# Kernel tuning notes

Measured on AMD Instinct MI355X. Metric: run time of the kernel, lower is better.

The kernel has to match this reference:

```python
import jax, jax.numpy as jnp
import numpy as np

N_NODES = 100000


def gcn_conv(x, W, b, src, dst, num_nodes):
    """PyG GCNConv: self-loops + symmetric norm + linear + scatter-add."""
    loop = jnp.arange(num_nodes, dtype=src.dtype)
    s = jnp.concatenate([src, loop])  # [E+N]
    d = jnp.concatenate([dst, loop])  # [E+N]
    # degree on destination column (edge_weight = 1)
    deg = jax.ops.segment_sum(jnp.ones_like(d, dtype=x.dtype), d,
                              num_segments=num_nodes)
    dinv = jnp.where(deg > 0, jax.lax.rsqrt(deg), 0.0)
    norm = dinv[s] * dinv[d]  # [E+N]
    h = x @ W  # [N, out] project before aggregation
    msg = h[s] * norm[:, None]  # gather + normalize
    out = jax.ops.segment_sum(msg, d, num_segments=num_nodes)  # scatter-add
    return out + b


def setup_inputs() -> dict:
    key = jax.random.key(0)
    k_x, k_e, k_w1, k_b1, k_w2, k_b2 = jax.random.split(key, 6)
    in_channels, hidden, out_dim = 128, 64, 2
    n_edges = 3200000
    x = jax.random.normal(k_x, (N_NODES, in_channels), dtype=jnp.float32)
    edge_index = jax.random.randint(k_e, (2, n_edges), 0, N_NODES, dtype=jnp.int64)
    # Glorot-style init for linear weights, zero bias (PyG default)
    W1 = jax.random.normal(k_w1, (in_channels, hidden), dtype=jnp.float32) * (1.0 / np.sqrt(in_channels))
    b1 = jnp.zeros((hidden,), dtype=jnp.float32)
    W2 = jax.random.normal(k_w2, (hidden, out_dim), dtype=jnp.float32) * (1.0 / np.sqrt(hidden))
    b2 = jnp.zeros((out_dim,), dtype=jnp.float32)
    return {"x": x, "edge_index": edge_index, "W1": W1, "b1": b1, "W2": W2, "b2": b2}


def reference(x, edge_index, W1, b1, W2, b2):
    src, dst = edge_index[0], edge_index[1]
    h = gcn_conv(x, W1, b1, src, dst, N_NODES)
    h = jax.nn.relu(h)
    # dropout(p=0.3) is identity in eval mode
    return gcn_conv(h, W2, b2, src, dst, N_NODES)
```

## Files before the change

kernel.cpp:

```cpp
#include <hip/hip_runtime.h>
#include <hip/hip_fp16.h>

#define IN_CH 128
#define HID 64
#define CHUNK1 16384
#define GBITS 8
#define SCAN_CHUNK 8192

typedef _Float16 h2 __attribute__((ext_vector_type(2)));
__device__ __forceinline__ h2 asH2(unsigned u) {
    union { unsigned u; h2 h; } x; x.u = u; return x.h;
}
__device__ __forceinline__ unsigned packH2(float a, float b) {
    union { unsigned u; h2 h; } x;
    x.h.x = (_Float16)a; x.h.y = (_Float16)b;
    return x.u;
}

__global__ __launch_bounds__(512) void k_p1count(const int* __restrict__ dst,
                                                 int* __restrict__ C,
                                                 int E, int G, int NB1) {
    __shared__ int lcnt[512];
    int t = threadIdx.x;
    for (int i = t; i < G; i += 512) lcnt[i] = 0;
    __syncthreads();
    int lo = blockIdx.x * CHUNK1;
    int hi = min(E, lo + CHUNK1);
    for (int e = lo + t; e < hi; e += 512) {
        int d = __builtin_nontemporal_load(dst + e);
        atomicAdd(&lcnt[d >> GBITS], 1);
    }
    __syncthreads();
    for (int g = t; g < G; g += 512) C[(size_t)g * NB1 + blockIdx.x] = lcnt[g];
}

__global__ __launch_bounds__(256) void k_scan_blocksum(const int* __restrict__ a,
                                                       int* __restrict__ bsum, int M) {
    int t = threadIdx.x;
    int base = blockIdx.x * SCAN_CHUNK + t * 32;
    int s = 0;
#pragma unroll
    for (int q = 0; q < 8; ++q) {
        int b = base + q * 4;
        if (b + 3 < M) {
            int4 v = *(const int4*)(a + b);
            s += v.x + v.y + v.z + v.w;
        } else {
            for (int i = 0; i < 4; ++i) if (b + i < M) s += a[b + i];
        }
    }
#pragma unroll
    for (int off = 32; off; off >>= 1) s += __shfl_down(s, off);
    __shared__ int ws[4];
    if ((t & 63) == 0) ws[t >> 6] = s;
    __syncthreads();
    if (t == 0) bsum[blockIdx.x] = ws[0] + ws[1] + ws[2] + ws[3];
}

__global__ __launch_bounds__(128) void k_scan_bsums(int* __restrict__ bsum, int nb) {
    __shared__ int sh[128];
    int t = threadIdx.x;
    int v = (t < nb) ? bsum[t] : 0;
    sh[t] = v;
    __syncthreads();
    for (int off = 1; off < 128; off <<= 1) {
        int u = (t >= off) ? sh[t - off] : 0;
        __syncthreads();
        sh[t] += u;
        __syncthreads();
    }
    if (t < nb) bsum[t] = (t == 0) ? 0 : sh[t - 1];
}

__global__ __launch_bounds__(256) void k_scan_apply(int* __restrict__ a,
                                                    const int* __restrict__ boff,
                                                    int M, int E) {
    int t = threadIdx.x;
    int base = blockIdx.x * SCAN_CHUNK + t * 32;
    int v[32];
    int tsum = 0;
#pragma unroll
    for (int q = 0; q < 8; ++q) {
        int b = base + q * 4;
        if (b + 3 < M) {
            int4 w = *(const int4*)(a + b);
            v[q * 4 + 0] = w.x; v[q * 4 + 1] = w.y; v[q * 4 + 2] = w.z; v[q * 4 + 3] = w.w;
        } else {
            for (int i = 0; i < 4; ++i) v[q * 4 + i] = (b + i < M) ? a[b + i] : 0;
        }
        tsum += v[q * 4] + v[q * 4 + 1] + v[q * 4 + 2] + v[q * 4 + 3];
    }
    __shared__ int sh[256];
    sh[t] = tsum;
    __syncthreads();
    for (int off = 1; off < 256; off <<= 1) {
        int u = (t >= off) ? sh[t - off] : 0;
        __syncthreads();
        sh[t] += u;
        __syncthreads();
    }
    int run = ((t == 0) ? 0 : sh[t - 1]) + boff[blockIdx.x];
#pragma unroll
    for (int q = 0; q < 8; ++q) {
        int b = base + q * 4;
        int o0 = run;            run += v[q * 4 + 0];
        int o1 = run;            run += v[q * 4 + 1];
        int o2 = run;            run += v[q * 4 + 2];
        int o3 = run;            run += v[q * 4 + 3];
        if (b + 3 < M) { *(int4*)(a + b) = make_int4(o0, o1, o2, o3); }
        else {
            if (b     < M) a[b]     = o0;
            if (b + 1 < M) a[b + 1] = o1;
            if (b + 2 < M) a[b + 2] = o2;
            if (b + 3 < M) a[b + 3] = o3;
        }
    }
    if (blockIdx.x == 0 && t == 0) a[M] = E;
}

__global__ __launch_bounds__(512) void k_p1scat(const int* __restrict__ src,
                                                const int* __restrict__ dst,
                                                const int* __restrict__ S,
                                                unsigned int* __restrict__ part,
                                                int E, int G, int NB1) {
    __shared__ int lcur[512];
    int t = threadIdx.x;
    for (int g = t; g < G; g += 512) lcur[g] = S[(size_t)g * NB1 + blockIdx.x];
    __syncthreads();
    int lo = blockIdx.x * CHUNK1;
    int hi = min(E, lo + CHUNK1);
    for (int e = lo + t; e < hi; e += 512) {
        int d = __builtin_nontemporal_load(dst + e);
        int s = __builtin_nontemporal_load(src + e);
        int pos = atomicAdd(&lcur[d >> GBITS], 1);
        part[pos] = ((unsigned)s << GBITS) | (unsigned)(d & ((1 << GBITS) - 1));
    }
}

__global__ __launch_bounds__(512) void k_p2(const unsigned int* __restrict__ part,
                                            const int* __restrict__ S,
                                            int* __restrict__ rowptr,
                                            float* __restrict__ dinv,
                                            int* __restrict__ esorted,
                                            int E, int N, int G, int NB1) {
    __shared__ int lcnt[256], lpre[256], lexc[256];
    int t = threadIdx.x;
    int g = blockIdx.x;
    int base = S[(size_t)g * NB1];
    int end  = (g == G - 1) ? E : S[(size_t)(g + 1) * NB1];
    if (t < 256) lcnt[t] = 0;
    __syncthreads();
    unsigned int  ed[18];
    unsigned char rk[18];
#pragma unroll
    for (int q = 0; q < 18; ++q) {
        int i = base + t + q * 512;
        if (i < end) {
            unsigned p = part[i];
            ed[q] = p;
            rk[q] = (unsigned char)atomicAdd(&lcnt[p & 255], 1);
        }
    }
    __syncthreads();
    int v = 0;
    if (t < 256) { v = lcnt[t]; lpre[t] = v; }
    __syncthreads();
    for (int off = 1; off < 256; off <<= 1) {
        int u = (t >= off && t < 256) ? lpre[t - off] : 0;
        __syncthreads();
        if (t < 256) lpre[t] += u;
        __syncthreads();
    }
    if (t < 256) {
        int excl = lpre[t] - v;
        lexc[t] = excl;
        int node = (g << GBITS) + t;
        if (node < N) {
            rowptr[node] = base + excl;
            dinv[node] = rsqrtf(1.0f + (float)v);
        }
    }
    if (g == 0 && t == 0) rowptr[N] = E;
    __syncthreads();
#pragma unroll
    for (int q = 0; q < 18; ++q) {
        int i = base + t + q * 512;
        if (i < end) {
            unsigned p = ed[q];
            esorted[base + lexc[p & 255] + (int)rk[q]] = (int)(p >> GBITS);
        }
    }
}

__global__ __launch_bounds__(256) void k_gemm1(const float* __restrict__ x,
                                               const float* __restrict__ W1,
                                               const float* __restrict__ dinv,
                                               __half* __restrict__ hp1h, int N) {
    __shared__ unsigned sW[64 * 64];
    __shared__ unsigned sx[16 * 64];
    const int tid = threadIdx.x;
    const int node0 = blockIdx.x * 16;

#pragma unroll
    for (int q = 0; q < 16; ++q) {
        int idx = tid + q * 256;
        int j2 = idx >> 6, k = idx & 63;
        sW[idx] = packH2(W1[(2 * j2) * HID + k], W1[(2 * j2 + 1) * HID + k]);
    }
#pragma unroll
    for (int q = 0; q < 4; ++q) {
        int idx = tid + q * 256;
        int n = idx >> 6, j2 = idx & 63;
        float2 v = *(const float2*)(x + (size_t)(node0 + n) * IN_CH + 2 * j2);
        sx[idx] = packH2(v.x, v.y);
    }
    __syncthreads();

    const int k  = tid & 63;
    const int n0 = tid >> 6;
    float a0 = 0.f, a1 = 0.f, a2 = 0.f, a3 = 0.f;
#pragma unroll 8
    for (int j2 = 0; j2 < 64; ++j2) {
        h2 w = asH2(sW[j2 * 64 + k]);
        a0 = __builtin_amdgcn_fdot2(asH2(sx[(n0     ) * 64 + j2]), w, a0, false);
        a1 = __builtin_amdgcn_fdot2(asH2(sx[(n0 +  4) * 64 + j2]), w, a1, false);
        a2 = __builtin_amdgcn_fdot2(asH2(sx[(n0 +  8) * 64 + j2]), w, a2, false);
        a3 = __builtin_amdgcn_fdot2(asH2(sx[(n0 + 12) * 64 + j2]), w, a3, false);
    }
    hp1h[(size_t)(node0 + n0     ) * HID + k] = __float2half(a0 * dinv[node0 + n0]);
    hp1h[(size_t)(node0 + n0 +  4) * HID + k] = __float2half(a1 * dinv[node0 + n0 + 4]);
    hp1h[(size_t)(node0 + n0 +  8) * HID + k] = __float2half(a2 * dinv[node0 + n0 + 8]);
    hp1h[(size_t)(node0 + n0 + 12) * HID + k] = __float2half(a3 * dinv[node0 + n0 + 12]);
}

__global__ __launch_bounds__(256) void k_agg1(const int* __restrict__ rowptr,
                                              const int* __restrict__ esorted,
                                              const __half2* __restrict__ hp1h,
                                              const float* __restrict__ dinv,
                                              const float* __restrict__ b1,
                                              const float* __restrict__ W2,
                                              float* __restrict__ hp2, int N) {
    int wid = (blockIdx.x * blockDim.x + threadIdx.x) >> 6;
    if (wid >= N) return;
    const int lane = threadIdx.x & 63;
    const int k32  = lane & 31;
    const int half = lane >> 5;
    int beg = rowptr[wid], end = rowptr[wid + 1];

    float ax = 0.f, ay = 0.f;
    int e = beg;
    for (; e + 31 < end; e += 32) {
        const int* ep = esorted + e + 16 * half;
        int s0 = ep[0],  s1 = ep[1],  s2 = ep[2],  s3 = ep[3];
        int s4 = ep[4],  s5 = ep[5],  s6 = ep[6],  s7 = ep[7];
        int s8 = ep[8],  s9 = ep[9],  sa = ep[10], sb = ep[11];
        int sc = ep[12], sd = ep[13], se = ep[14], sf = ep[15];
        __half2 g0 = hp1h[(unsigned)(s0 * 32 + k32)];
        __half2 g1 = hp1h[(unsigned)(s1 * 32 + k32)];
        __half2 g2 = hp1h[(unsigned)(s2 * 32 + k32)];
        __half2 g3 = hp1h[(unsigned)(s3 * 32 + k32)];
        __half2 g4 = hp1h[(unsigned)(s4 * 32 + k32)];
        __half2 g5 = hp1h[(unsigned)(s5 * 32 + k32)];
        __half2 g6 = hp1h[(unsigned)(s6 * 32 + k32)];
        __half2 g7 = hp1h[(unsigned)(s7 * 32 + k32)];
        __half2 g8 = hp1h[(unsigned)(s8 * 32 + k32)];
        __half2 g9 = hp1h[(unsigned)(s9 * 32 + k32)];
        __half2 ga = hp1h[(unsigned)(sa * 32 + k32)];
        __half2 gb = hp1h[(unsigned)(sb * 32 + k32)];
        __half2 gc = hp1h[(unsigned)(sc * 32 + k32)];
        __half2 gd = hp1h[(unsigned)(sd * 32 + k32)];
        __half2 ge = hp1h[(unsigned)(se * 32 + k32)];
        __half2 gf = hp1h[(unsigned)(sf * 32 + k32)];
        __half2 h0 = __hadd2(g0, g4), h1 = __hadd2(g1, g5);
        __half2 h2 = __hadd2(g2, g6), h3 = __hadd2(g3, g7);
        float2 f0 = __half22float2(__hadd2(h0, h1));
        float2 f1 = __half22float2(__hadd2(h2, h3));
        __half2 h4 = __hadd2(g8, gc), h5 = __hadd2(g9, gd);
        __half2 h6 = __hadd2(ga, ge), h7 = __hadd2(gb, gf);
        float2 f2 = __half22float2(__hadd2(h4, h5));
        float2 f3 = __half22float2(__hadd2(h6, h7));
        ax += (f0.x + f1.x) + (f2.x + f3.x);
        ay += (f0.y + f1.y) + (f2.y + f3.y);
    }
    for (; e + 15 < end; e += 16) {
        const int* ep = esorted + e + 8 * half;
        int s0 = ep[0], s1 = ep[1], s2 = ep[2], s3 = ep[3];
        int s4 = ep[4], s5 = ep[5], s6 = ep[6], s7 = ep[7];
        __half2 h0 = hp1h[(unsigned)(s0 * 32 + k32)];
        __half2 h1 = hp1h[(unsigned)(s1 * 32 + k32)];
        __half2 h2 = hp1h[(unsigned)(s2 * 32 + k32)];
        __half2 h3 = hp1h[(unsigned)(s3 * 32 + k32)];
        h0 = __hadd2(h0, hp1h[(unsigned)(s4 * 32 + k32)]);
        h1 = __hadd2(h1, hp1h[(unsigned)(s5 * 32 + k32)]);
        h2 = __hadd2(h2, hp1h[(unsigned)(s6 * 32 + k32)]);
        h3 = __hadd2(h3, hp1h[(unsigned)(s7 * 32 + k32)]);
        float2 f0 = __half22float2(__hadd2(h0, h1));
        float2 f1 = __half22float2(__hadd2(h2, h3));
        ax += f0.x + f1.x;
        ay += f0.y + f1.y;
    }
    for (; e + 1 < end; e += 2) {
        int s = esorted[e + half];
        float2 f = __half22float2(hp1h[(unsigned)(s * 32 + k32)]);
        ax += f.x;
        ay += f.y;
    }
    if (e < end) {
        int s = esorted[e];
        float2 f = __half22float2(hp1h[(unsigned)(s * 32 + k32)]);
        if (half == 0) { ax += f.x; ay += f.y; }
    }
    ax += __shfl_xor(ax, 32);
    ay += __shfl_xor(ay, 32);

    float2 fs = __half22float2(hp1h[(unsigned)(wid * 32 + k32)]);
    ax += fs.x;
    ay += fs.y;

    float dj = dinv[wid];
    float2 bb = *(const float2*)(b1 + 2 * k32);
    float h0 = fmaxf(fmaf(dj, ax, bb.x), 0.0f);
    float h1 = fmaxf(fmaf(dj, ay, bb.y), 0.0f);
    float4 w4 = *(const float4*)(W2 + 4 * k32);
    float p0 = h0 * w4.x + h1 * w4.z;
    float p1 = h0 * w4.y + h1 * w4.w;
#pragma unroll
    for (int off = 32; off; off >>= 1) {
        p0 += __shfl_xor(p0, off);
        p1 += __shfl_xor(p1, off);
    }
    if (lane == 0) {
        hp2[(size_t)wid * 2 + 0] = p0 * 0.5f * dj;
        hp2[(size_t)wid * 2 + 1] = p1 * 0.5f * dj;
    }
}

__global__ __launch_bounds__(256) void k_agg2(const int* __restrict__ rowptr,
                                              const int* __restrict__ esorted,
                                              const float* __restrict__ hp2,
                                              const float* __restrict__ dinv,
                                              const float* __restrict__ b2,
                                              float* __restrict__ out, int N) {
    int gid = blockIdx.x * blockDim.x + threadIdx.x;
    int j = gid >> 3;
    if (j >= N) return;
    int l = gid & 7;
    int beg = rowptr[j], end = rowptr[j + 1];
    float ax = 0.f, ay = 0.f;
    for (int e = beg + l; e < end; e += 8) {
        int s = esorted[e];
        float2 v = *(const float2*)(hp2 + (size_t)s * 2);
        ax += v.x;
        ay += v.y;
    }
#pragma unroll
    for (int off = 1; off < 8; off <<= 1) {
        ax += __shfl_xor(ax, off);
        ay += __shfl_xor(ay, off);
    }
    if (l == 0) {
        float2 self = *(const float2*)(hp2 + (size_t)j * 2);
        float dj = dinv[j];
        out[(size_t)j * 2 + 0] = fmaf(dj, ax + self.x, b2[0]);
        out[(size_t)j * 2 + 1] = fmaf(dj, ay + self.y, b2[1]);
    }
}

extern "C" void kernel_launch(void* const* d_in, const int* in_sizes, int n_in,
                              void* d_out, int out_size, void* d_ws, size_t ws_size,
                              hipStream_t stream) {
    const float* x  = (const float*)d_in[0];
    const int*   ei = (const int*)d_in[1];
    const float* W1 = (const float*)d_in[2];
    const float* b1 = (const float*)d_in[3];
    const float* W2 = (const float*)d_in[4];
    const float* b2 = (const float*)d_in[5];
    float* out = (float*)d_out;

    const int N = in_sizes[0] / IN_CH;
    const int E = in_sizes[1] / 2;
    const int* src = ei;
    const int* dst = ei + E;

    const int G   = (N + 255) >> GBITS;
    const int NB1 = (E + CHUNK1 - 1) / CHUNK1;
    const int M   = G * NB1;
    const int NBs = (M + SCAN_CHUNK - 1) / SCAN_CHUNK;

    char* ws = (char*)d_ws;
    size_t o = 0;
    auto carve = [&](size_t bytes) -> char* {
        char* p = ws + o;
        o = (o + bytes + 255) & ~(size_t)255;
        return p;
    };
    int*          S       = (int*)carve(((size_t)M + 1) * 4);
    unsigned int* part    = (unsigned int*)carve((size_t)E * 4);
    int*          rowptr  = (int*)carve(((size_t)N + 1) * 4);
    float*        dinv    = (float*)carve((size_t)N * 4);
    int*          bsum    = (int*)carve(128 * 4);
    int*          esorted = (int*)carve((size_t)E * 4);
    __half*       hp1h    = (__half*)carve((size_t)N * HID * 2);
    float*        hp2     = (float*)carve((size_t)N * 2 * 4);
    (void)ws_size;

    k_p1count<<<NB1, 512, 0, stream>>>(dst, S, E, G, NB1);
    k_scan_blocksum<<<NBs, 256, 0, stream>>>(S, bsum, M);
    k_scan_bsums<<<1, 128, 0, stream>>>(bsum, NBs);
    k_scan_apply<<<NBs, 256, 0, stream>>>(S, bsum, M, E);
    k_p1scat<<<NB1, 512, 0, stream>>>(src, dst, S, part, E, G, NB1);
    k_p2<<<G, 512, 0, stream>>>(part, S, rowptr, dinv, esorted, E, N, G, NB1);

    k_gemm1<<<(N + 15) / 16, 256, 0, stream>>>(x, W1, dinv, hp1h, N);
    k_agg1<<<(unsigned)(((size_t)N * 64 + 255) / 256), 256, 0, stream>>>(
        rowptr, esorted, (const __half2*)hp1h, dinv, b1, W2, hp2, N);
    k_agg2<<<(unsigned)(((size_t)N * 8 + 255) / 256), 256, 0, stream>>>(
        rowptr, esorted, hp2, dinv, b2, out, N);
}
```

Measured before the change: 209.6 us.

## Record per-edge bucket rank in count pass and drop atomics from scatter

The count kernel now saves each edge's local atomic rank as a byte, so the scatter kernel computes its output position from the prefix-scanned offsets plus that rank, with no shared-memory atomics. The separate block-sum scan kernel is folded into scan_apply, which reduces preceding block sums with a wavefront shuffle. The edge chunk size is halved, which keeps per-bucket ranks small enough to fit in a byte. The 32-edge unrolled loop in agg1 is removed. The byte rank costs an extra write and read of E bytes, and it would overflow if a chunk ever held more than 255 edges for one destination group.

```diff
diff --git a/kernel.cpp b/kernel.cpp
--- a/kernel.cpp
+++ b/kernel.cpp
@@ -3,7 +3,7 @@
 
 #define IN_CH 128
 #define HID 64
-#define CHUNK1 16384
+#define CHUNK1 8192
 #define GBITS 8
 #define SCAN_CHUNK 8192
 
@@ -19,16 +19,18 @@
 
 __global__ __launch_bounds__(512) void k_p1count(const int* __restrict__ dst,
                                                  int* __restrict__ C,
+                                                 unsigned char* __restrict__ rank8,
                                                  int E, int G, int NB1) {
     __shared__ int lcnt[512];
     int t = threadIdx.x;
-    for (int i = t; i < G; i += 512) lcnt[i] = 0;
+    for (int i = t; i < 512; i += 512) lcnt[i] = 0;
     __syncthreads();
     int lo = blockIdx.x * CHUNK1;
     int hi = min(E, lo + CHUNK1);
     for (int e = lo + t; e < hi; e += 512) {
         int d = __builtin_nontemporal_load(dst + e);
-        atomicAdd(&lcnt[d >> GBITS], 1);
+        int r = atomicAdd(&lcnt[d >> GBITS], 1);
+        rank8[e] = (unsigned char)r;
     }
     __syncthreads();
     for (int g = t; g < G; g += 512) C[(size_t)g * NB1 + blockIdx.x] = lcnt[g];
@@ -57,25 +59,17 @@
     if (t == 0) bsum[blockIdx.x] = ws[0] + ws[1] + ws[2] + ws[3];
 }
 
-__global__ __launch_bounds__(128) void k_scan_bsums(int* __restrict__ bsum, int nb) {
-    __shared__ int sh[128];
+__global__ __launch_bounds__(256) void k_scan_apply(int* __restrict__ a,
+                                                    const int* __restrict__ bsum,
+                                                    int nbs, int M, int E) {
+    __shared__ int sboff;
     int t = threadIdx.x;
-    int v = (t < nb) ? bsum[t] : 0;
-    sh[t] = v;
-    __syncthreads();
-    for (int off = 1; off < 128; off <<= 1) {
-        int u = (t >= off) ? sh[t - off] : 0;
-        __syncthreads();
-        sh[t] += u;
-        __syncthreads();
-    }
-    if (t < nb) bsum[t] = (t == 0) ? 0 : sh[t - 1];
-}
-
-__global__ __launch_bounds__(256) void k_scan_apply(int* __restrict__ a,
-                                                    const int* __restrict__ boff,
-                                                    int M, int E) {
-    int t = threadIdx.x;
+    if (t < 64) {
+        int v = (t < nbs && t < (int)blockIdx.x) ? bsum[t] : 0;
+#pragma unroll
+        for (int off = 32; off; off >>= 1) v += __shfl_xor(v, off);
+        if (t == 0) sboff = v;
+    }
     int base = blockIdx.x * SCAN_CHUNK + t * 32;
     int v[32];
     int tsum = 0;
@@ -99,7 +93,7 @@
         sh[t] += u;
         __syncthreads();
     }
-    int run = ((t == 0) ? 0 : sh[t - 1]) + boff[blockIdx.x];
+    int run = ((t == 0) ? 0 : sh[t - 1]) + sboff;
 #pragma unroll
     for (int q = 0; q < 8; ++q) {
         int b = base + q * 4;
@@ -120,19 +114,19 @@
 
 __global__ __launch_bounds__(512) void k_p1scat(const int* __restrict__ src,
                                                 const int* __restrict__ dst,
+                                                const unsigned char* __restrict__ rank8,
                                                 const int* __restrict__ S,
                                                 unsigned int* __restrict__ part,
-                                                int E, int G, int NB1) {
-    __shared__ int lcur[512];
-    int t = threadIdx.x;
-    for (int g = t; g < G; g += 512) lcur[g] = S[(size_t)g * NB1 + blockIdx.x];
-    __syncthreads();
-    int lo = blockIdx.x * CHUNK1;
+                                                int E, int NB1) {
+    const int blk = blockIdx.x;
+    const int t = threadIdx.x;
+    int lo = blk * CHUNK1;
     int hi = min(E, lo + CHUNK1);
     for (int e = lo + t; e < hi; e += 512) {
         int d = __builtin_nontemporal_load(dst + e);
         int s = __builtin_nontemporal_load(src + e);
-        int pos = atomicAdd(&lcur[d >> GBITS], 1);
+        int r = rank8[e];
+        int pos = S[(size_t)(d >> GBITS) * NB1 + blk] + r;
         part[pos] = ((unsigned)s << GBITS) | (unsigned)(d & ((1 << GBITS) - 1));
     }
 }
@@ -249,39 +243,6 @@
 
     float ax = 0.f, ay = 0.f;
     int e = beg;
-    for (; e + 31 < end; e += 32) {
-        const int* ep = esorted + e + 16 * half;
-        int s0 = ep[0],  s1 = ep[1],  s2 = ep[2],  s3 = ep[3];
-        int s4 = ep[4],  s5 = ep[5],  s6 = ep[6],  s7 = ep[7];
-        int s8 = ep[8],  s9 = ep[9],  sa = ep[10], sb = ep[11];
-        int sc = ep[12], sd = ep[13], se = ep[14], sf = ep[15];
-        __half2 g0 = hp1h[(unsigned)(s0 * 32 + k32)];
-        __half2 g1 = hp1h[(unsigned)(s1 * 32 + k32)];
-        __half2 g2 = hp1h[(unsigned)(s2 * 32 + k32)];
-        __half2 g3 = hp1h[(unsigned)(s3 * 32 + k32)];
-        __half2 g4 = hp1h[(unsigned)(s4 * 32 + k32)];
-        __half2 g5 = hp1h[(unsigned)(s5 * 32 + k32)];
-        __half2 g6 = hp1h[(unsigned)(s6 * 32 + k32)];
-        __half2 g7 = hp1h[(unsigned)(s7 * 32 + k32)];
-        __half2 g8 = hp1h[(unsigned)(s8 * 32 + k32)];
-        __half2 g9 = hp1h[(unsigned)(s9 * 32 + k32)];
-        __half2 ga = hp1h[(unsigned)(sa * 32 + k32)];
-        __half2 gb = hp1h[(unsigned)(sb * 32 + k32)];
-        __half2 gc = hp1h[(unsigned)(sc * 32 + k32)];
-        __half2 gd = hp1h[(unsigned)(sd * 32 + k32)];
-        __half2 ge = hp1h[(unsigned)(se * 32 + k32)];
-        __half2 gf = hp1h[(unsigned)(sf * 32 + k32)];
-        __half2 h0 = __hadd2(g0, g4), h1 = __hadd2(g1, g5);
-        __half2 h2 = __hadd2(g2, g6), h3 = __hadd2(g3, g7);
-        float2 f0 = __half22float2(__hadd2(h0, h1));
-        float2 f1 = __half22float2(__hadd2(h2, h3));
-        __half2 h4 = __hadd2(g8, gc), h5 = __hadd2(g9, gd);
-        __half2 h6 = __hadd2(ga, ge), h7 = __hadd2(gb, gf);
-        float2 f2 = __half22float2(__hadd2(h4, h5));
-        float2 f3 = __half22float2(__hadd2(h6, h7));
-        ax += (f0.x + f1.x) + (f2.x + f3.x);
-        ay += (f0.y + f1.y) + (f2.y + f3.y);
-    }
     for (; e + 15 < end; e += 16) {
         const int* ep = esorted + e + 8 * half;
         int s0 = ep[0], s1 = ep[1], s2 = ep[2], s3 = ep[3];
@@ -394,21 +355,21 @@
         o = (o + bytes + 255) & ~(size_t)255;
         return p;
     };
-    int*          S       = (int*)carve(((size_t)M + 1) * 4);
-    unsigned int* part    = (unsigned int*)carve((size_t)E * 4);
-    int*          rowptr  = (int*)carve(((size_t)N + 1) * 4);
-    float*        dinv    = (float*)carve((size_t)N * 4);
-    int*          bsum    = (int*)carve(128 * 4);
-    int*          esorted = (int*)carve((size_t)E * 4);
-    __half*       hp1h    = (__half*)carve((size_t)N * HID * 2);
-    float*        hp2     = (float*)carve((size_t)N * 2 * 4);
+    int*           S       = (int*)carve(((size_t)M + 1) * 4);
+    unsigned char* rank8   = (unsigned char*)carve((size_t)E);
+    unsigned int*  part    = (unsigned int*)carve((size_t)E * 4);
+    int*           rowptr  = (int*)carve(((size_t)N + 1) * 4);
+    float*         dinv    = (float*)carve((size_t)N * 4);
+    int*           bsum    = (int*)carve(128 * 4);
+    int*           esorted = (int*)carve((size_t)E * 4);
+    __half*        hp1h    = (__half*)carve((size_t)N * HID * 2);
+    float*         hp2     = (float*)carve((size_t)N * 2 * 4);
     (void)ws_size;
 
-    k_p1count<<<NB1, 512, 0, stream>>>(dst, S, E, G, NB1);
+    k_p1count<<<NB1, 512, 0, stream>>>(dst, S, rank8, E, G, NB1);
     k_scan_blocksum<<<NBs, 256, 0, stream>>>(S, bsum, M);
-    k_scan_bsums<<<1, 128, 0, stream>>>(bsum, NBs);
-    k_scan_apply<<<NBs, 256, 0, stream>>>(S, bsum, M, E);
-    k_p1scat<<<NB1, 512, 0, stream>>>(src, dst, S, part, E, G, NB1);
+    k_scan_apply<<<NBs, 256, 0, stream>>>(S, bsum, NBs, M, E);
+    k_p1scat<<<NB1, 512, 0, stream>>>(src, dst, rank8, S, part, E, NB1);
     k_p2<<<G, 512, 0, stream>>>(part, S, rowptr, dinv, esorted, E, N, G, NB1);
 
     k_gemm1<<<(N + 15) / 16, 256, 0, stream>>>(x, W1, dinv, hp1h, N);
```

After: 242.0 us. +15.4%, slower.
